# Optimization experiments

Hardware: AMD Instinct MI355X
Metric: run time of the kernel (lower is better)

The kernel has to match this reference:

```python
import jax, jax.numpy as jnp
import numpy as np

FEATURE_DIM = 128
N_NODES = 100000
N_EDGES = 800000
L1_IN = 2 * FEATURE_DIM            # 256
L1_OUT = int((2 * FEATURE_DIM) ** 0.5)  # 16
L2_DIM = L1_OUT + 1                # 17


def leaky(x):
    return jnp.where(x >= 0, x, 0.1 * x)


def setup_inputs() -> dict:
    key = jax.random.key(0)
    ks = jax.random.split(key, 8)
    Jt_ind = jax.random.randint(ks[0], (2, N_EDGES), 0, N_NODES)
    Jt_val = jax.random.normal(ks[1], (N_EDGES,), dtype=jnp.float32)
    f = jax.random.normal(ks[2], (N_NODES, FEATURE_DIM), dtype=jnp.float32)
    W1 = jax.random.normal(ks[3], (L1_IN, L1_OUT), dtype=jnp.float32) * (1.0 / np.sqrt(L1_IN))
    b1 = jnp.zeros((L1_OUT,), dtype=jnp.float32)
    W2 = jax.random.normal(ks[4], (L2_DIM, L2_DIM), dtype=jnp.float32) * (1.0 / np.sqrt(L2_DIM))
    b2 = jnp.zeros((L2_DIM,), dtype=jnp.float32)
    Wc = jax.random.normal(ks[5], (L2_DIM, 1), dtype=jnp.float32) * (1.0 / np.sqrt(L2_DIM))
    bc = jnp.ones((1,), dtype=jnp.float32)  # collapse_bias = 1
    return {"Jt_ind": Jt_ind, "Jt_val": Jt_val, "f": f, "N": N_NODES,
            "W1": W1, "b1": b1, "W2": W2, "b2": b2, "Wc": Wc, "bc": bc}


def reference(Jt_ind, Jt_val, f, N, W1, b1, W2, b2, Wc, bc):
    i = Jt_ind[0]
    j = Jt_ind[1]
    absv = jnp.abs(Jt_val)                                     # [E]
    # degree: per-destination sum of |Jt_val|
    deg_abs = jax.ops.segment_sum(absv, i, num_segments=N)     # [N]
    Jt_val_abs_norm = absv / deg_abs[i]                        # [E]
    # gather endpoint features and run tiny edge-MLP
    x = jnp.concatenate([f[i], f[j]], axis=1)                  # [E, 2F]
    x = leaky(x @ W1 + b1)                                     # [E, L1_OUT]
    x = jnp.concatenate([x, Jt_val_abs_norm[:, None]], axis=1) # [E, L2_DIM]
    x = leaky(x @ W2 + b2)                                     # [E, L2_DIM]
    e_values = (x @ Wc + bc)[:, 0]                             # [E]
    # segment softmax over edges grouped by destination i (stable)
    m = jax.ops.segment_max(e_values, i, num_segments=N)       # [N]
    ex = jnp.exp(e_values - m[i])                              # [E]
    s = jax.ops.segment_sum(ex, i, num_segments=N)             # [N]
    return ex / s[i]                                           # [E]
```

## Files before the change

kernel.cpp:

```cpp
#include <hip/hip_runtime.h>
#include <hip/hip_fp16.h>
#include <math.h>

#define FDIM  128
#define L1OUT 16
#define L2DIM 17
#define TRM   128
#define HSTR  136

typedef _Float16 f16x8 __attribute__((ext_vector_type(8)));
typedef float    f32x4 __attribute__((ext_vector_type(4)));

struct __align__(16) H16 { __half2 h[8]; };

__device__ __forceinline__ float lrelu(float v) { return v >= 0.f ? v : 0.1f * v; }

__global__ void node_transform(
    const float* __restrict__ f, const float* __restrict__ W1,
    const float* __restrict__ b1,
    const int* __restrict__ ind_i, const float* __restrict__ val,
    H16* __restrict__ A, H16* __restrict__ B,
    float* __restrict__ deg, int N, int E)
{
    __shared__ __align__(16) _Float16 tile[TRM * HSTR];

    const int t    = threadIdx.x;
    const int gtid = blockIdx.x * 256 + t;
    const int GT   = gridDim.x * 256;

    {
        const int E4 = E >> 2;
        for (int q = gtid; q < E4; q += GT) {
            int e = q << 2;
            int4   ii = *reinterpret_cast<const int4*>(ind_i + e);
            float4 vv = *reinterpret_cast<const float4*>(val + e);
            atomicAdd(&deg[ii.x], fabsf(vv.x));
            atomicAdd(&deg[ii.y], fabsf(vv.y));
            atomicAdd(&deg[ii.z], fabsf(vv.z));
            atomicAdd(&deg[ii.w], fabsf(vv.w));
        }
        if (gtid < (E & 3)) {
            int e = (E & ~3) + gtid;
            atomicAdd(&deg[ind_i[e]], fabsf(val[e]));
        }
    }

    const int lane = t & 63;
    const int wv   = t >> 6;
    const int n    = lane & 15;
    const int quad = lane >> 4;

    f16x8 bfr[2][4];
#pragma unroll
    for (int nt = 0; nt < 2; ++nt)
#pragma unroll
        for (int ks = 0; ks < 4; ++ks) {
            f16x8 bf;
#pragma unroll
            for (int j = 0; j < 8; ++j) {
                int k = 32 * ks + 8 * quad + j;
                bf[j] = (_Float16)W1[(size_t)(nt * FDIM + k) * L1OUT + n];
            }
            bfr[nt][ks] = bf;
        }
    float b1v = b1[n];

    const int base = blockIdx.x * TRM;
#pragma unroll
    for (int q = 0; q < 8; ++q) {
        int p  = t + 256 * q;
        int r  = p >> 4;
        int c8 = p & 15;
        float4 lo = make_float4(0.f, 0.f, 0.f, 0.f);
        float4 hi = lo;
        if (base + r < N) {
            const float4* src = reinterpret_cast<const float4*>(
                f + (size_t)(base + r) * FDIM + c8 * 8);
            lo = src[0];
            hi = src[1];
        }
        f16x8 hx;
        hx[0] = (_Float16)lo.x; hx[1] = (_Float16)lo.y;
        hx[2] = (_Float16)lo.z; hx[3] = (_Float16)lo.w;
        hx[4] = (_Float16)hi.x; hx[5] = (_Float16)hi.y;
        hx[6] = (_Float16)hi.z; hx[7] = (_Float16)hi.w;
        *reinterpret_cast<f16x8*>(&tile[r * HSTR + c8 * 8]) = hx;
    }
    __syncthreads();

#pragma unroll
    for (int si = 0; si < 2; ++si) {
        const int m0 = (wv + 4 * si) * 16;
        f32x4 acc0 = { b1v, b1v, b1v, b1v };
        f32x4 acc1 = { 0.f, 0.f, 0.f, 0.f };
#pragma unroll
        for (int ks = 0; ks < 4; ++ks) {
            f16x8 af = *reinterpret_cast<const f16x8*>(
                &tile[(m0 + n) * HSTR + 32 * ks + 8 * quad]);
            acc0 = __builtin_amdgcn_mfma_f32_16x16x32_f16(af, bfr[0][ks], acc0, 0, 0, 0);
            acc1 = __builtin_amdgcn_mfma_f32_16x16x32_f16(af, bfr[1][ks], acc1, 0, 0, 0);
        }
#pragma unroll
        for (int reg = 0; reg < 4; ++reg) {
            int node = base + m0 + quad * 4 + reg;
            if (node < N) {
                reinterpret_cast<_Float16*>(A + node)[n] = (_Float16)acc0[reg];
                reinterpret_cast<_Float16*>(B + node)[n] = (_Float16)acc1[reg];
            }
        }
    }
}

#define MLP_TAIL(X, EXOUT)                                                  \
    {                                                                       \
        float acc[L2DIM];                                                   \
        _Pragma("unroll")                                                   \
        for (int r = 0; r < L2DIM; ++r) acc[r] = b2s[r];                    \
        _Pragma("unroll")                                                   \
        for (int c = 0; c < L2DIM; ++c) {                                   \
            float xc = X[c];                                                \
            const float4* r4 = reinterpret_cast<const float4*>(&w2s[c * 20]); \
            float4 w0 = r4[0], w1v = r4[1], w2v = r4[2], w3 = r4[3];        \
            float  w16 = w2s[c * 20 + 16];                                  \
            acc[0]  += xc * w0.x;  acc[1]  += xc * w0.y;                    \
            acc[2]  += xc * w0.z;  acc[3]  += xc * w0.w;                    \
            acc[4]  += xc * w1v.x; acc[5]  += xc * w1v.y;                   \
            acc[6]  += xc * w1v.z; acc[7]  += xc * w1v.w;                   \
            acc[8]  += xc * w2v.x; acc[9]  += xc * w2v.y;                   \
            acc[10] += xc * w2v.z; acc[11] += xc * w2v.w;                   \
            acc[12] += xc * w3.x;  acc[13] += xc * w3.y;                    \
            acc[14] += xc * w3.z;  acc[15] += xc * w3.w;                    \
            acc[16] += xc * w16;                                            \
        }                                                                   \
        float ev = bc0s;                                                    \
        _Pragma("unroll")                                                   \
        for (int r = 0; r < L2DIM; ++r) ev += lrelu(acc[r]) * wcs[r];       \
        EXOUT = __expf(ev);                                                 \
    }

__global__ __launch_bounds__(256, 4) void edge_mlp(
    const int* __restrict__ ind, const float* __restrict__ val,
    const H16* __restrict__ A, const H16* __restrict__ B,
    const float* __restrict__ deg,
    const float* __restrict__ W2, const float* __restrict__ b2,
    const float* __restrict__ Wc, const float* __restrict__ bc,
    float* __restrict__ eout, float* __restrict__ ssum, int E)
{
    __shared__ float w2s[L2DIM * 20];
    __shared__ float b2s[L2DIM];
    __shared__ float wcs[L2DIM];
    __shared__ float bc0s;

    const int t = threadIdx.x;
    for (int idx = t; idx < L2DIM * L2DIM; idx += 256) {
        int c = idx / L2DIM, r = idx - c * L2DIM;
        w2s[c * 20 + r] = W2[idx];
    }
    if (t < L2DIM) b2s[t] = b2[t];
    if (t < L2DIM) wcs[t] = Wc[t];
    if (t == 0)    bc0s   = bc[0];
    __syncthreads();

    const int E2 = (E + 1) >> 1;
    const int p  = blockIdx.x * 256 + t;
    if (p >= E2) return;

    const int  e0   = p;
    const int  e1   = p + E2;
    const bool has1 = (e1 < E);
    const int  e1s  = has1 ? e1 : e0;

    int i0 = ind[e0];   int j0 = ind[E + e0];
    int i1 = ind[e1s];  int j1 = ind[E + e1s];

    const f16x8* pA0 = reinterpret_cast<const f16x8*>(A + i0);
    const f16x8* pB0 = reinterpret_cast<const f16x8*>(B + j0);
    const f16x8* pA1 = reinterpret_cast<const f16x8*>(A + i1);
    const f16x8* pB1 = reinterpret_cast<const f16x8*>(B + j1);

    f16x8 a0lo = pA0[0], a0hi = pA0[1];
    f16x8 b0lo = pB0[0], b0hi = pB0[1];
    float v0   = val[e0];
    float d0   = deg[i0];
    f16x8 a1lo = pA1[0], a1hi = pA1[1];
    f16x8 b1lo = pB1[0], b1hi = pB1[1];
    float v1   = val[e1s];
    float d1   = deg[i1];

    {
        float x[L2DIM];
#pragma unroll
        for (int k = 0; k < 8; ++k) {
            x[k]     = lrelu((float)a0lo[k] + (float)b0lo[k]);
            x[k + 8] = lrelu((float)a0hi[k] + (float)b0hi[k]);
        }
        x[L1OUT] = fabsf(v0) / d0;
        float ex0;
        MLP_TAIL(x, ex0);
        eout[e0] = ex0;
        atomicAdd(&ssum[i0], ex0);
    }

    if (has1) {
        float x[L2DIM];
#pragma unroll
        for (int k = 0; k < 8; ++k) {
            x[k]     = lrelu((float)a1lo[k] + (float)b1lo[k]);
            x[k + 8] = lrelu((float)a1hi[k] + (float)b1hi[k]);
        }
        x[L1OUT] = fabsf(v1) / d1;
        float ex1;
        MLP_TAIL(x, ex1);
        eout[e1] = ex1;
        atomicAdd(&ssum[i1], ex1);
    }
}

__global__ void normalize(const int* __restrict__ ind_i, const float* __restrict__ ssum,
                          float* __restrict__ ex, int E) {
    int t = blockIdx.x * blockDim.x + threadIdx.x;
    int e = t * 4;
    if (e + 3 < E) {
        int4   ii = *reinterpret_cast<const int4*>(ind_i + e);
        float4 vv = *reinterpret_cast<const float4*>(ex + e);
        vv.x /= ssum[ii.x];
        vv.y /= ssum[ii.y];
        vv.z /= ssum[ii.z];
        vv.w /= ssum[ii.w];
        *reinterpret_cast<float4*>(ex + e) = vv;
    } else {
        for (; e < E; ++e) ex[e] = ex[e] / ssum[ind_i[e]];
    }
}

extern "C" void kernel_launch(void* const* d_in, const int* in_sizes, int n_in,
                              void* d_out, int out_size, void* d_ws, size_t ws_size,
                              hipStream_t stream) {
    const int*   Jt_ind = (const int*)  d_in[0];
    const float* Jt_val = (const float*)d_in[1];
    const float* f      = (const float*)d_in[2];
    const float* W1 = (const float*)d_in[4];
    const float* b1 = (const float*)d_in[5];
    const float* W2 = (const float*)d_in[6];
    const float* b2 = (const float*)d_in[7];
    const float* Wc = (const float*)d_in[8];
    const float* bc = (const float*)d_in[9];

    const int E = in_sizes[1];
    const int N = in_sizes[2] / FDIM;
    float* out = (float*)d_out;

    char* ws = (char*)d_ws;
    float* deg  = (float*)ws;  ws += (size_t)N * sizeof(float);
    float* ssum = (float*)ws;  ws += (size_t)N * sizeof(float);
    H16*   A    = (H16*)ws;    ws += (size_t)N * sizeof(H16);
    H16*   Bm   = (H16*)ws;    ws += (size_t)N * sizeof(H16);

    const int B256 = 256;
    const int nblk = (N + TRM - 1) / TRM;
    const int E2   = (E + 1) / 2;
    const int eblk = (E2 + B256 - 1) / B256;
    const int qblk = ((E + 3) / 4 + B256 - 1) / B256;

    hipMemsetAsync(deg, 0, 2 * (size_t)N * sizeof(float), stream);
    node_transform<<<nblk, B256, 0, stream>>>(f, W1, b1, Jt_ind, Jt_val,
                                              A, Bm, deg, N, E);
    edge_mlp      <<<eblk, B256, 0, stream>>>(Jt_ind, Jt_val, A, Bm, deg,
                                              W2, b2, Wc, bc, out, ssum, E);
    normalize     <<<qblk, B256, 0, stream>>>(Jt_ind, ssum, out, E);
}
```

Baseline: 209.6 us.

## Fuse edge MLP and softmax normalize via cooperative grid sync; drop LDS staging

```diff
diff --git a/kernel.cpp b/kernel.cpp
--- a/kernel.cpp
+++ b/kernel.cpp
@@ -1,4 +1,5 @@
 #include <hip/hip_runtime.h>
+#include <hip/hip_cooperative_groups.h>
 #include <hip/hip_fp16.h>
 #include <math.h>
 
@@ -6,7 +7,8 @@
 #define L1OUT 16
 #define L2DIM 17
 #define TRM   128
-#define HSTR  136
+
+namespace cg = cooperative_groups;
 
 typedef _Float16 f16x8 __attribute__((ext_vector_type(8)));
 typedef float    f32x4 __attribute__((ext_vector_type(4)));
@@ -15,15 +17,13 @@
 
 __device__ __forceinline__ float lrelu(float v) { return v >= 0.f ? v : 0.1f * v; }
 
-__global__ void node_transform(
+__global__ __launch_bounds__(256, 6) void node_transform(
     const float* __restrict__ f, const float* __restrict__ W1,
     const float* __restrict__ b1,
     const int* __restrict__ ind_i, const float* __restrict__ val,
     H16* __restrict__ A, H16* __restrict__ B,
     float* __restrict__ deg, int N, int E)
 {
-    __shared__ __align__(16) _Float16 tile[TRM * HSTR];
-
     const int t    = threadIdx.x;
     const int gtid = blockIdx.x * 256 + t;
     const int GT   = gridDim.x * 256;
@@ -66,37 +66,26 @@
     float b1v = b1[n];
 
     const int base = blockIdx.x * TRM;
-#pragma unroll
-    for (int q = 0; q < 8; ++q) {
-        int p  = t + 256 * q;
-        int r  = p >> 4;
-        int c8 = p & 15;
-        float4 lo = make_float4(0.f, 0.f, 0.f, 0.f);
-        float4 hi = lo;
-        if (base + r < N) {
-            const float4* src = reinterpret_cast<const float4*>(
-                f + (size_t)(base + r) * FDIM + c8 * 8);
-            lo = src[0];
-            hi = src[1];
-        }
-        f16x8 hx;
-        hx[0] = (_Float16)lo.x; hx[1] = (_Float16)lo.y;
-        hx[2] = (_Float16)lo.z; hx[3] = (_Float16)lo.w;
-        hx[4] = (_Float16)hi.x; hx[5] = (_Float16)hi.y;
-        hx[6] = (_Float16)hi.z; hx[7] = (_Float16)hi.w;
-        *reinterpret_cast<f16x8*>(&tile[r * HSTR + c8 * 8]) = hx;
-    }
-    __syncthreads();
 
 #pragma unroll
     for (int si = 0; si < 2; ++si) {
         const int m0 = (wv + 4 * si) * 16;
+        int row = base + m0 + n;
+        if (row > N - 1) row = N - 1;
+        const float* fr = f + (size_t)row * FDIM;
+
         f32x4 acc0 = { b1v, b1v, b1v, b1v };
         f32x4 acc1 = { 0.f, 0.f, 0.f, 0.f };
 #pragma unroll
         for (int ks = 0; ks < 4; ++ks) {
-            f16x8 af = *reinterpret_cast<const f16x8*>(
-                &tile[(m0 + n) * HSTR + 32 * ks + 8 * quad]);
+            const float4* p = reinterpret_cast<const float4*>(fr + 32 * ks + 8 * quad);
+            float4 lo = p[0];
+            float4 hi = p[1];
+            f16x8 af;
+            af[0] = (_Float16)lo.x; af[1] = (_Float16)lo.y;
+            af[2] = (_Float16)lo.z; af[3] = (_Float16)lo.w;
+            af[4] = (_Float16)hi.x; af[5] = (_Float16)hi.y;
+            af[6] = (_Float16)hi.z; af[7] = (_Float16)hi.w;
             acc0 = __builtin_amdgcn_mfma_f32_16x16x32_f16(af, bfr[0][ks], acc0, 0, 0, 0);
             acc1 = __builtin_amdgcn_mfma_f32_16x16x32_f16(af, bfr[1][ks], acc1, 0, 0, 0);
         }
@@ -138,6 +127,117 @@
         EXOUT = __expf(ev);                                                 \
     }
 
+#define EDGE_X(X, ALO, AHI, BLO, BHI, V, D)                                 \
+    _Pragma("unroll")                                                       \
+    for (int k = 0; k < 8; ++k) {                                           \
+        X[k]     = lrelu((float)ALO[k] + (float)BLO[k]);                    \
+        X[k + 8] = lrelu((float)AHI[k] + (float)BHI[k]);                    \
+    }                                                                       \
+    X[L1OUT] = fabsf(V) / D;
+
+__global__ __launch_bounds__(256, 4) void edge_mlp_norm(
+    const int* __restrict__ ind, const float* __restrict__ val,
+    const H16* __restrict__ A, const H16* __restrict__ B,
+    const float* __restrict__ deg,
+    const float* __restrict__ W2, const float* __restrict__ b2,
+    const float* __restrict__ Wc, const float* __restrict__ bc,
+    float* __restrict__ out, float* __restrict__ ssum, int E, int NT)
+{
+    __shared__ float w2s[L2DIM * 20];
+    __shared__ float b2s[L2DIM];
+    __shared__ float wcs[L2DIM];
+    __shared__ float bc0s;
+
+    const int t = threadIdx.x;
+    for (int idx = t; idx < L2DIM * L2DIM; idx += 256) {
+        int c = idx / L2DIM, r = idx - c * L2DIM;
+        w2s[c * 20 + r] = W2[idx];
+    }
+    if (t < L2DIM) b2s[t] = b2[t];
+    if (t < L2DIM) wcs[t] = Wc[t];
+    if (t == 0)    bc0s   = bc[0];
+    __syncthreads();
+
+    const int tid = blockIdx.x * 256 + t;
+    const int Em  = E - 1;
+    const int e0 = tid, e1 = tid + NT, e2 = tid + 2 * NT, e3 = tid + 3 * NT;
+    const bool h0 = e0 < E, h1 = e1 < E, h2 = e2 < E, h3 = e3 < E;
+    const int s0 = h0 ? e0 : Em, s1 = h1 ? e1 : Em,
+              s2 = h2 ? e2 : Em, s3 = h3 ? e3 : Em;
+
+    int   i0, i1, i2, i3;
+    float ex0 = 0.f, ex1 = 0.f, ex2 = 0.f, ex3 = 0.f;
+
+    i0 = ind[s0];  int j0 = ind[E + s0];
+    i1 = ind[s1];  int j1 = ind[E + s1];
+    {
+        const f16x8* pA0 = reinterpret_cast<const f16x8*>(A + i0);
+        const f16x8* pB0 = reinterpret_cast<const f16x8*>(B + j0);
+        const f16x8* pA1 = reinterpret_cast<const f16x8*>(A + i1);
+        const f16x8* pB1 = reinterpret_cast<const f16x8*>(B + j1);
+        f16x8 a0lo = pA0[0], a0hi = pA0[1];
+        f16x8 b0lo = pB0[0], b0hi = pB0[1];
+        float v0   = val[s0];
+        float d0   = deg[i0];
+        f16x8 a1lo = pA1[0], a1hi = pA1[1];
+        f16x8 b1lo = pB1[0], b1hi = pB1[1];
+        float v1   = val[s1];
+        float d1   = deg[i1];
+        {
+            float x[L2DIM];
+            EDGE_X(x, a0lo, a0hi, b0lo, b0hi, v0, d0);
+            MLP_TAIL(x, ex0);
+        }
+        if (h0) atomicAdd(&ssum[i0], ex0);
+        {
+            float x[L2DIM];
+            EDGE_X(x, a1lo, a1hi, b1lo, b1hi, v1, d1);
+            MLP_TAIL(x, ex1);
+        }
+        if (h1) atomicAdd(&ssum[i1], ex1);
+    }
+
+    i2 = ind[s2];  int j2 = ind[E + s2];
+    i3 = ind[s3];  int j3 = ind[E + s3];
+    {
+        const f16x8* pA2 = reinterpret_cast<const f16x8*>(A + i2);
+        const f16x8* pB2 = reinterpret_cast<const f16x8*>(B + j2);
+        const f16x8* pA3 = reinterpret_cast<const f16x8*>(A + i3);
+        const f16x8* pB3 = reinterpret_cast<const f16x8*>(B + j3);
+        f16x8 a2lo = pA2[0], a2hi = pA2[1];
+        f16x8 b2lo = pB2[0], b2hi = pB2[1];
+        float v2   = val[s2];
+        float d2   = deg[i2];
+        f16x8 a3lo = pA3[0], a3hi = pA3[1];
+        f16x8 b3lo = pB3[0], b3hi = pB3[1];
+        float v3   = val[s3];
+        float d3   = deg[i3];
+        {
+            float x[L2DIM];
+            EDGE_X(x, a2lo, a2hi, b2lo, b2hi, v2, d2);
+            MLP_TAIL(x, ex2);
+        }
+        if (h2) atomicAdd(&ssum[i2], ex2);
+        {
+            float x[L2DIM];
+            EDGE_X(x, a3lo, a3hi, b3lo, b3hi, v3, d3);
+            MLP_TAIL(x, ex3);
+        }
+        if (h3) atomicAdd(&ssum[i3], ex3);
+    }
+
+    cg::this_grid().sync();
+
+    float S0 = __hip_atomic_load(&ssum[i0], __ATOMIC_RELAXED, __HIP_MEMORY_SCOPE_AGENT);
+    float S1 = __hip_atomic_load(&ssum[i1], __ATOMIC_RELAXED, __HIP_MEMORY_SCOPE_AGENT);
+    float S2 = __hip_atomic_load(&ssum[i2], __ATOMIC_RELAXED, __HIP_MEMORY_SCOPE_AGENT);
+    float S3 = __hip_atomic_load(&ssum[i3], __ATOMIC_RELAXED, __HIP_MEMORY_SCOPE_AGENT);
+    if (h0) out[e0] = ex0 / S0;
+    if (h1) out[e1] = ex1 / S1;
+    if (h2) out[e2] = ex2 / S2;
+    if (h3) out[e3] = ex3 / S3;
+}
+
 __global__ __launch_bounds__(256, 4) void edge_mlp(
     const int* __restrict__ ind, const float* __restrict__ val,
     const H16* __restrict__ A, const H16* __restrict__ B,
@@ -189,26 +289,15 @@
 
     {
         float x[L2DIM];
-#pragma unroll
-        for (int k = 0; k < 8; ++k) {
-            x[k]     = lrelu((float)a0lo[k] + (float)b0lo[k]);
-            x[k + 8] = lrelu((float)a0hi[k] + (float)b0hi[k]);
-        }
-        x[L1OUT] = fabsf(v0) / d0;
+        EDGE_X(x, a0lo, a0hi, b0lo, b0hi, v0, d0);
         float ex0;
         MLP_TAIL(x, ex0);
         eout[e0] = ex0;
         atomicAdd(&ssum[i0], ex0);
     }
-
     if (has1) {
         float x[L2DIM];
-#pragma unroll
-        for (int k = 0; k < 8; ++k) {
-            x[k]     = lrelu((float)a1lo[k] + (float)b1lo[k]);
-            x[k + 8] = lrelu((float)a1hi[k] + (float)b1hi[k]);
-        }
-        x[L1OUT] = fabsf(v1) / d1;
+        EDGE_X(x, a1lo, a1hi, b1lo, b1hi, v1, d1);
         float ex1;
         MLP_TAIL(x, ex1);
         eout[e1] = ex1;
@@ -258,14 +347,38 @@
 
     const int B256 = 256;
     const int nblk = (N + TRM - 1) / TRM;
-    const int E2   = (E + 1) / 2;
-    const int eblk = (E2 + B256 - 1) / B256;
-    const int qblk = ((E + 3) / 4 + B256 - 1) / B256;
 
     hipMemsetAsync(deg, 0, 2 * (size_t)N * sizeof(float), stream);
     node_transform<<<nblk, B256, 0, stream>>>(f, W1, b1, Jt_ind, Jt_val,
                                               A, Bm, deg, N, E);
-    edge_mlp      <<<eblk, B256, 0, stream>>>(Jt_ind, Jt_val, A, Bm, deg,
-                                              W2, b2, Wc, bc, out, ssum, E);
-    normalize     <<<qblk, B256, 0, stream>>>(Jt_ind, ssum, out, E);
-}
+
+    hipError_t cerr = hipErrorUnknown;
+    int cblk = (E + 4 * B256 - 1) / (4 * B256);
+    if (cblk < 1) cblk = 1;
+    if (cblk <= 1024) {
+        int NT = cblk * B256;
+        const int*   ind_a  = Jt_ind;
+        const float* val_a  = Jt_val;
+        const H16*   A_a    = A;
+        const H16*   B_a    = Bm;
+        const float* deg_a  = deg;
+        float*       out_a  = out;
+        float*       ssum_a = ssum;
+        int          E_a    = E;
+        int          NT_a   = NT;
+        void* args[] = { (void*)&ind_a, (void*)&val_a, (void*)&A_a, (void*)&B_a,
+                         (void*)&deg_a, (void*)&W2, (void*)&b2, (void*)&Wc,
+                         (void*)&bc, (void*)&out_a, (void*)&ssum_a,
+                         (void*)&E_a, (void*)&NT_a };
+        cerr = hipLaunchCooperativeKernel((void*)edge_mlp_norm, dim3(cblk),
+                                          dim3(B256), args, 0, stream);
+    }
+    if (cerr != hipSuccess) {
+        const int E2   = (E + 1) / 2;
+        const int eblk = (E2 + B256 - 1) / B256;
+        const int qblk = ((E + 3) / 4 + B256 - 1) / B256;
+        edge_mlp <<<eblk, B256, 0, stream>>>(Jt_ind, Jt_val, A, Bm, deg,
+                                             W2, b2, Wc, bc, out, ssum, E);
+        normalize<<<qblk, B256, 0, stream>>>(Jt_ind, ssum, out, E);
+    }
+}
```

After: 353.7 us. +68.8%, slower.
